# Optimization experiments

Hardware: AMD Instinct MI355X
Metric: run time of the kernel (lower is better)

Reference implementation:

```python
import jax, jax.numpy as jnp
import numpy as np

D = 256; NH = 8; NL = 4; NP = 4; HD = D // NH
SHAPES = [(128, 128), (64, 64), (32, 32), (16, 16)]
S = sum(h * w for h, w in SHAPES)  # 21760
B = 2; Q = 10000


def setup_inputs() -> dict:
    key = jax.random.key(0)
    ks = jax.random.split(key, 12)
    sc = 0.02
    return {
        "query": jax.random.normal(ks[0], (B, Q, D), jnp.float32),
        "ref_points": jax.random.uniform(ks[1], (B, Q, NL, 2), jnp.float32),
        "value": jax.random.normal(ks[2], (B, S, D), jnp.float32),
        "spatial_shapes": np.array(SHAPES, dtype=np.int64),
        "Wv": jax.random.normal(ks[3], (D, D), jnp.float32) * sc,
        "bv": jnp.zeros((D,), jnp.float32),
        "Ws": jax.random.normal(ks[4], (D, NH * NL * NP * 2), jnp.float32) * sc,
        "bs": jax.random.normal(ks[5], (NH * NL * NP * 2,), jnp.float32) * 0.5,
        "Wa": jax.random.normal(ks[6], (D, NH * NL * NP), jnp.float32) * sc,
        "ba": jnp.zeros((NH * NL * NP,), jnp.float32),
        "Wo": jax.random.normal(ks[7], (D, D), jnp.float32) * sc,
        "bo": jnp.zeros((D,), jnp.float32),
    }


def _ms_deform_attn(query, ref_points, value, shapes, Wv, bv, Ws, bs, Wa, ba, Wo, bo):
    Bn, Qn, _ = query.shape
    # value projection -> [B, NH, S, HD]
    v = (value @ Wv + bv).reshape(Bn, -1, NH, HD).transpose(0, 2, 1, 3)
    # sampling offsets [B,Q,NH,NL,NP,2] and softmax attn weights [B,Q,NH,NL,NP]
    off = (query @ Ws + bs).reshape(Bn, Qn, NH, NL, NP, 2)
    w = jax.nn.softmax((query @ Wa + ba).reshape(Bn, Qn, NH, NL * NP), axis=-1)
    w = w.reshape(Bn, Qn, NH, NL, NP)
    # per-level [w, h] normalizer (note original builds [[w,h] for h,w in shapes])
    norm = jnp.array([[wd, ht] for ht, wd in shapes], dtype=query.dtype)
    locs = ref_points[:, :, None, :, None, :] + off / norm[None, None, None, :, None, :]
    grids = (2.0 * locs - 1.0).transpose(0, 2, 1, 3, 4, 5)  # [B,NH,Q,NL,NP,2]
    wt = w.transpose(0, 2, 1, 3, 4)                          # [B,NH,Q,NL,NP]

    out = jnp.zeros((Bn, NH, Qn, HD), query.dtype)
    start = 0
    for lid, (h, wd) in enumerate(shapes):
        vl = v[:, :, start:start + h * wd, :]  # [B,NH,h*w,HD]
        g = grids[:, :, :, lid]                # [B,NH,Q,NP,2]
        # torch grid_sample align_corners=False pixel coords
        x = ((g[..., 0] + 1.0) * wd - 1.0) * 0.5
        y = ((g[..., 1] + 1.0) * h - 1.0) * 0.5
        x0f = jnp.floor(x); y0f = jnp.floor(y)
        lx = x - x0f; ly = y - y0f
        x0 = x0f.astype(jnp.int32); y0 = y0f.astype(jnp.int32)

        def samp(iy, ix):
            valid = ((iy >= 0) & (iy < h) & (ix >= 0) & (ix < wd)).astype(vl.dtype)
            idx = jnp.clip(iy, 0, h - 1) * wd + jnp.clip(ix, 0, wd - 1)  # [B,NH,Q,NP]
            flat = idx.reshape(Bn, NH, Qn * NP)
            gathered = jnp.take_along_axis(vl, flat[..., None], axis=2)
            return gathered.reshape(Bn, NH, Qn, NP, HD) * valid[..., None]

        s = (samp(y0, x0) * ((1 - lx) * (1 - ly))[..., None]
             + samp(y0, x0 + 1) * (lx * (1 - ly))[..., None]
             + samp(y0 + 1, x0) * ((1 - lx) * ly)[..., None]
             + samp(y0 + 1, x0 + 1) * (lx * ly)[..., None])
        out = out + jnp.einsum('bnqph,bnqp->bnqh', s, wt[:, :, :, lid])
        start += h * wd

    out = out.transpose(0, 2, 1, 3).reshape(Bn, Qn, D)
    return out @ Wo + bo


def reference(query, ref_points, value, spatial_shapes, Wv, bv, Ws, bs, Wa, ba, Wo, bo):
    shapes = [(int(h), int(w)) for h, w in np.asarray(spatial_shapes)]
    return _ms_deform_attn(query, ref_points, value, shapes, Wv, bv, Ws, bs, Wa, ba, Wo, bo)
```

## Files before the change

### kernel.cpp

```cpp
#include <hip/hip_runtime.h>

#define NB_B  2
#define NB_Q  10000
#define NB_D  256
#define NB_NH 8
#define NB_NL 4
#define NB_NP 4
#define NB_HD 32
#define NB_S  21760
#define MQ    20000
#define MQB   313
#define NVB   1360
#define NCB   939

#define ASTR  536
#define BSTR  1048

typedef _Float16 half8 __attribute__((ext_vector_type(8)));
typedef float f32x4 __attribute__((ext_vector_type(4)));

__global__ __launch_bounds__(256) void k_prepw(const float* __restrict__ Wv,
                                               const float* __restrict__ Ws,
                                               const float* __restrict__ Wa,
                                               const float* __restrict__ Wo,
                                               _Float16* __restrict__ Wvt,
                                               _Float16* __restrict__ Wsat,
                                               _Float16* __restrict__ Wot)
{
    const int k = threadIdx.x;
    const int nc = blockIdx.x;
    if (nc < 256) {
        Wvt[nc * 256 + k] = (_Float16)Wv[k * 256 + nc];
    } else if (nc < 640) {
        const int n = nc - 256;
        const float v = (n < 256) ? Ws[k * 256 + n] : Wa[k * 128 + (n - 256)];
        Wsat[n * 256 + k] = (_Float16)v;
    } else {
        const int n = nc - 640;
        Wot[n * 256 + k] = (_Float16)Wo[k * 256 + n];
    }
}

__global__ __launch_bounds__(256) void k_front(const float* __restrict__ value,
                                               const float* __restrict__ query,
                                               const _Float16* __restrict__ Wvt,
                                               const _Float16* __restrict__ Wsat,
                                               const float* __restrict__ refp,
                                               const float* __restrict__ bv,
                                               const float* __restrict__ bs,
                                               const float* __restrict__ ba,
                                               _Float16* __restrict__ vt,
                                               float* __restrict__ sx,
                                               float* __restrict__ sy,
                                               float* __restrict__ sw)
{
    __shared__ __align__(16) _Float16 Ah[2][4 * ASTR];
    __shared__ __align__(16) _Float16 Bh[2][4 * BSTR];
    __shared__ float rp[64][8];

    const int t = threadIdx.x;
    const int lane = t & 63, w = t >> 6;
    const int bid = blockIdx.x;
    const bool isv = (bid < NVB);

    int row0, n0;
    const float* Asrc;
    const _Float16* Bsrc;
    if (isv) {
        n0 = (bid & 1) * 128;
        row0 = (bid >> 1) * 64;
        Asrc = value;
        Bsrc = Wvt;
    } else {
        const int cid = bid - NVB;
        n0 = (cid % 3) * 128;
        row0 = (cid / 3) * 64;
        Asrc = query;
        Bsrc = Wsat;
        const int i0 = row0 * 8 + t;
        rp[t >> 3][t & 7] = refp[min(i0, MQ * 8 - 1)];
        const int i1 = i0 + 256;
        rp[32 + (t >> 3)][t & 7] = refp[min(i1, MQ * 8 - 1)];
    }

    const int arr = t >> 3;
    const int acl = t & 7;
    const int bnn = t >> 2;
    const int bcl = t & 3;

    const float* gA0;
    const float* gA1;
    {
        int r0i = row0 + arr, r1i = row0 + 32 + arr;
        if (!isv) { r0i = min(r0i, MQ - 1); r1i = min(r1i, MQ - 1); }
        gA0 = Asrc + (size_t)r0i * 256 + acl * 4;
        gA1 = Asrc + (size_t)r1i * 256 + acl * 4;
    }
    const _Float16* gB0 = Bsrc + (size_t)(n0 + bnn) * 256 + bcl * 8;
    const _Float16* gB1 = Bsrc + (size_t)(n0 + 64 + bnn) * 256 + bcl * 8;

    float4 ar0, ar1;
    uint4  br0, br1;
#define LOADT(kt) { ar0 = *reinterpret_cast<const float4*>(gA0 + (kt) * 32); \
                    ar1 = *reinterpret_cast<const float4*>(gA1 + (kt) * 32); \
                    br0 = *reinterpret_cast<const uint4*>(gB0 + (kt) * 32);  \
                    br1 = *reinterpret_cast<const uint4*>(gB1 + (kt) * 32); }

    LOADT(0);

    f32x4 acc[4][2];
#pragma unroll
    for (int fr = 0; fr < 4; ++fr)
#pragma unroll
        for (int fc = 0; fc < 2; ++fc) acc[fr][fc] = (f32x4){0.f, 0.f, 0.f, 0.f};

    const int rowb = lane & 15;
    const int kq = lane >> 4;
    const int awoff = (acl >> 1) * ASTR + arr * 8 + (acl & 1) * 4;
    int buf = 0;
#pragma unroll
    for (int kt = 0; kt < 8; ++kt) {
        {
            union { _Float16 h[4]; uint2 u; } p0, p1;
            p0.h[0] = (_Float16)ar0.x; p0.h[1] = (_Float16)ar0.y;
            p0.h[2] = (_Float16)ar0.z; p0.h[3] = (_Float16)ar0.w;
            p1.h[0] = (_Float16)ar1.x; p1.h[1] = (_Float16)ar1.y;
            p1.h[2] = (_Float16)ar1.z; p1.h[3] = (_Float16)ar1.w;
            *reinterpret_cast<uint2*>(&Ah[buf][awoff])           = p0.u;
            *reinterpret_cast<uint2*>(&Ah[buf][awoff + 32 * 8])  = p1.u;
            *reinterpret_cast<uint4*>(&Bh[buf][bcl * BSTR + bnn * 8])        = br0;
            *reinterpret_cast<uint4*>(&Bh[buf][bcl * BSTR + (64 + bnn) * 8]) = br1;
        }
        if (kt < 7) LOADT(kt + 1);
        __syncthreads();

        half8 af[4], bf[2];
#pragma unroll
        for (int fr = 0; fr < 4; ++fr)
            af[fr] = *reinterpret_cast<const half8*>(&Ah[buf][kq * ASTR + (fr * 16 + rowb) * 8]);
#pragma unroll
        for (int fc = 0; fc < 2; ++fc)
            bf[fc] = *reinterpret_cast<const half8*>(&Bh[buf][kq * BSTR + (w * 32 + fc * 16 + rowb) * 8]);
#pragma unroll
        for (int fr = 0; fr < 4; ++fr)
#pragma unroll
            for (int fc = 0; fc < 2; ++fc)
                acc[fr][fc] = __builtin_amdgcn_mfma_f32_16x16x32_f16(af[fr], bf[fc], acc[fr][fc], 0, 0, 0);
        buf ^= 1;
    }
#undef LOADT

    if (isv) {
        const int b = (row0 >= NB_S) ? 1 : 0;
        const int sb = row0 - b * NB_S;
#pragma unroll
        for (int fc = 0; fc < 2; ++fc) {
            const int n = n0 + w * 32 + fc * 16 + rowb;
            const int h = n >> 5, hd = n & 31;
            const float bvn = bv[n];
#pragma unroll
            for (int fr = 0; fr < 4; ++fr) {
                const f32x4 c = acc[fr][fc];
#pragma unroll
                for (int j = 0; j < 4; ++j) {
                    const int m = fr * 16 + (lane >> 4) * 4 + j;
                    vt[((size_t)((b * NB_NH + h) * NB_S + (sb + m)) << 5) + hd] = (_Float16)(c[j] + bvn);
                }
            }
        }
    } else if (n0 < 256) {
#pragma unroll
        for (int fc = 0; fc < 2; ++fc) {
            const int n = n0 + w * 32 + fc * 16 + rowb;
            const int si = n >> 1, xy = n & 1;
            const int l = (n >> 3) & 3;
            const float dim = (float)(128 >> l);
            const float bsv = bs[n];
            float* dst = xy ? sy : sx;
#pragma unroll
            for (int fr = 0; fr < 4; ++fr) {
                const f32x4 c = acc[fr][fc];
#pragma unroll
                for (int j = 0; j < 4; ++j) {
                    const int m = fr * 16 + (lane >> 4) * 4 + j;
                    if (row0 + m < MQ) {
                        const float coord = rp[m][l * 2 + xy] * dim + (c[j] + bsv) - 0.5f;
                        dst[(size_t)(row0 + m) * 128 + si] = coord;
                    }
                }
            }
        }
    } else {
#pragma unroll
        for (int fc = 0; fc < 2; ++fc) {
            const int col = w * 32 + fc * 16 + rowb;
            const float bav = ba[col];
#pragma unroll
            for (int fr = 0; fr < 4; ++fr) {
                const f32x4 c = acc[fr][fc];
#pragma unroll
                for (int j = 0; j < 4; ++j) {
                    const int m = fr * 16 + (lane >> 4) * 4 + j;
                    float v = c[j] + bav;
                    float vm = v;
                    vm = fmaxf(vm, __shfl_xor(vm, 1));
                    vm = fmaxf(vm, __shfl_xor(vm, 2));
                    vm = fmaxf(vm, __shfl_xor(vm, 4));
                    vm = fmaxf(vm, __shfl_xor(vm, 8));
                    const float e = expf(v - vm);
                    float s = e;
                    s += __shfl_xor(s, 1);
                    s += __shfl_xor(s, 2);
                    s += __shfl_xor(s, 4);
                    s += __shfl_xor(s, 8);
                    if (row0 + m < MQ)
                        sw[(size_t)(row0 + m) * 128 + col] = e / s;
                }
            }
        }
    }
}

__global__ __launch_bounds__(256) void k_gather(const _Float16* __restrict__ vt,
                                                const float* __restrict__ sx,
                                                const float* __restrict__ sy,
                                                const float* __restrict__ sw,
                                                _Float16* __restrict__ tmp)
{
    __shared__ int   offs[16][16][4];
    __shared__ float wts[16][16][4];
    const int t = threadIdx.x;
    const int gid = blockIdx.x;
    const int h = gid & 7;
    const int row0 = (gid >> 3) * 16;
    const int b = (row0 >= NB_Q) ? 1 : 0;

    {
        const int r = t >> 4, s = t & 15;
        const size_t ci = (size_t)(row0 + r) * 128 + h * 16 + s;
        const float x = sx[ci], y = sy[ci], w = sw[ci];
        const int l = s >> 2;
        const int dim = 128 >> l;
        const int startL = (l == 0) ? 0 : (l == 1) ? 16384 : (l == 2) ? 20480 : 21504;
        const float x0f = floorf(x), y0f = floorf(y);
        const float lx = x - x0f, ly = y - y0f;
        const int ix = (int)x0f, iy = (int)y0f;
        const int ix0 = min(max(ix, 0), dim - 1), ix1 = min(max(ix + 1, 0), dim - 1);
        const int iy0 = min(max(iy, 0), dim - 1), iy1 = min(max(iy + 1, 0), dim - 1);
        const float vx0 = (ix >= 0 && ix < dim) ? 1.f : 0.f;
        const float vx1 = (ix + 1 >= 0 && ix + 1 < dim) ? 1.f : 0.f;
        const float vy0 = (iy >= 0 && iy < dim) ? 1.f : 0.f;
        const float vy1 = (iy + 1 >= 0 && iy + 1 < dim) ? 1.f : 0.f;
        offs[r][s][0] = (startL + iy0 * dim + ix0) * (NB_HD * 2);
        offs[r][s][1] = (startL + iy0 * dim + ix1) * (NB_HD * 2);
        offs[r][s][2] = (startL + iy1 * dim + ix0) * (NB_HD * 2);
        offs[r][s][3] = (startL + iy1 * dim + ix1) * (NB_HD * 2);
        wts[r][s][0] = w * (1.f - lx) * (1.f - ly) * vx0 * vy0;
        wts[r][s][1] = w * lx * (1.f - ly) * vx1 * vy0;
        wts[r][s][2] = w * (1.f - lx) * ly * vx0 * vy1;
        wts[r][s][3] = w * lx * ly * vx1 * vy1;
    }
    __syncthreads();

    const int r = t >> 4, hd2 = t & 15;
    const char* slab = reinterpret_cast<const char*>(vt)
                     + (size_t)(b * NB_NH + h) * NB_S * (NB_HD * 2);
    const int byo = hd2 * 4;
    float ax = 0.f, ay = 0.f;
#pragma unroll
    for (int s = 0; s < 16; ++s) {
        const int4   o = *reinterpret_cast<const int4*>(&offs[r][s][0]);
        const float4 w = *reinterpret_cast<const float4*>(&wts[r][s][0]);
        union { unsigned u; _Float16 h[2]; } c0, c1, c2, c3;
        c0.u = *reinterpret_cast<const unsigned*>(slab + (o.x + byo));
        c1.u = *reinterpret_cast<const unsigned*>(slab + (o.y + byo));
        c2.u = *reinterpret_cast<const unsigned*>(slab + (o.z + byo));
        c3.u = *reinterpret_cast<const unsigned*>(slab + (o.w + byo));
        ax = fmaf(w.x, (float)c0.h[0], ax); ay = fmaf(w.x, (float)c0.h[1], ay);
        ax = fmaf(w.y, (float)c1.h[0], ax); ay = fmaf(w.y, (float)c1.h[1], ay);
        ax = fmaf(w.z, (float)c2.h[0], ax); ay = fmaf(w.z, (float)c2.h[1], ay);
        ax = fmaf(w.w, (float)c3.h[0], ax); ay = fmaf(w.w, (float)c3.h[1], ay);
    }
    union { unsigned u; _Float16 h[2]; } p;
    p.h[0] = (_Float16)ax; p.h[1] = (_Float16)ay;
    *reinterpret_cast<unsigned*>(tmp + (size_t)(row0 + r) * 256 + h * 32 + hd2 * 2) = p.u;
}

__global__ __launch_bounds__(256) void k_oproj_mm(const _Float16* __restrict__ tmp,
                                                  const _Float16* __restrict__ Wot,
                                                  const float* __restrict__ bo,
                                                  float* __restrict__ out)
{
    __shared__ __align__(16) _Float16 Ao[2][4 * ASTR];
    __shared__ __align__(16) _Float16 Bh[2][4 * BSTR];
    const int t = threadIdx.x;
    const int lane = t & 63, w = t >> 6;
    const int bid = blockIdx.x;
    const int n0 = (bid & 1) * 128;
    const int row0 = (bid >> 1) * 64;

    const int arr = t >> 2;
    const int acl = t & 3;
    const int bnn = t >> 2;
    const int bcl = t & 3;

    const _Float16* gA0 = tmp + (size_t)min(row0 + arr, MQ - 1) * 256 + acl * 8;
    const _Float16* gB0 = Wot + (size_t)(n0 + bnn) * 256 + bcl * 8;
    const _Float16* gB1 = Wot + (size_t)(n0 + 64 + bnn) * 256 + bcl * 8;

    uint4 ar0, br0, br1;
#define LOADT(kt) { ar0 = *reinterpret_cast<const uint4*>(gA0 + (kt) * 32); \
                    br0 = *reinterpret_cast<const uint4*>(gB0 + (kt) * 32); \
                    br1 = *reinterpret_cast<const uint4*>(gB1 + (kt) * 32); }

    LOADT(0);

    f32x4 acc[4][2];
#pragma unroll
    for (int fr = 0; fr < 4; ++fr)
#pragma unroll
        for (int fc = 0; fc < 2; ++fc) acc[fr][fc] = (f32x4){0.f, 0.f, 0.f, 0.f};

    const int rowb = lane & 15;
    const int kq = lane >> 4;
    int buf = 0;
#pragma unroll
    for (int kt = 0; kt < 8; ++kt) {
        *reinterpret_cast<uint4*>(&Ao[buf][acl * ASTR + arr * 8])            = ar0;
        *reinterpret_cast<uint4*>(&Bh[buf][bcl * BSTR + bnn * 8])            = br0;
        *reinterpret_cast<uint4*>(&Bh[buf][bcl * BSTR + (64 + bnn) * 8])     = br1;
        if (kt < 7) LOADT(kt + 1);
        __syncthreads();

        half8 af[4], bf[2];
#pragma unroll
        for (int fr = 0; fr < 4; ++fr)
            af[fr] = *reinterpret_cast<const half8*>(&Ao[buf][kq * ASTR + (fr * 16 + rowb) * 8]);
#pragma unroll
        for (int fc = 0; fc < 2; ++fc)
            bf[fc] = *reinterpret_cast<const half8*>(&Bh[buf][kq * BSTR + (w * 32 + fc * 16 + rowb) * 8]);
#pragma unroll
        for (int fr = 0; fr < 4; ++fr)
#pragma unroll
            for (int fc = 0; fc < 2; ++fc)
                acc[fr][fc] = __builtin_amdgcn_mfma_f32_16x16x32_f16(af[fr], bf[fc], acc[fr][fc], 0, 0, 0);
        buf ^= 1;
    }
#undef LOADT

#pragma unroll
    for (int fc = 0; fc < 2; ++fc) {
        const int n = n0 + w * 32 + fc * 16 + rowb;
        const float bon = bo[n];
#pragma unroll
        for (int fr = 0; fr < 4; ++fr) {
            const f32x4 c = acc[fr][fc];
#pragma unroll
            for (int j = 0; j < 4; ++j) {
                const int m = fr * 16 + (lane >> 4) * 4 + j;
                if (row0 + m < MQ)
                    out[(size_t)(row0 + m) * 256 + n] = c[j] + bon;
            }
        }
    }
}

extern "C" void kernel_launch(void* const* d_in, const int* in_sizes, int n_in,
                              void* d_out, int out_size, void* d_ws, size_t ws_size,
                              hipStream_t stream)
{
    const float* query = (const float*)d_in[0];
    const float* refp  = (const float*)d_in[1];
    const float* value = (const float*)d_in[2];
    const float* Wv = (const float*)d_in[4];
    const float* bv = (const float*)d_in[5];
    const float* Ws = (const float*)d_in[6];
    const float* bs = (const float*)d_in[7];
    const float* Wa = (const float*)d_in[8];
    const float* ba = (const float*)d_in[9];
    const float* Wo = (const float*)d_in[10];
    const float* bo = (const float*)d_in[11];
    float* out = (float*)d_out;

    char* ws = (char*)d_ws;
    _Float16* vt_h  = (_Float16*)(ws + 0);
    _Float16* tmp_h = (_Float16*)(ws + 22282240);
    _Float16* Wvt   = (_Float16*)(ws + 32522240);
    _Float16* Wsat  = (_Float16*)(ws + 32653312);
    _Float16* Wot   = (_Float16*)(ws + 32849920);
    float*    sxg   = (float*)   (ws + 32980992);
    float*    syg   = (float*)   (ws + 43220992);
    float*    swg   = (float*)   (ws + 53460992);

    hipLaunchKernelGGL(k_prepw, dim3(896), dim3(256), 0, stream,
                       Wv, Ws, Wa, Wo, Wvt, Wsat, Wot);
    hipLaunchKernelGGL(k_front, dim3(NVB + NCB), dim3(256), 0, stream,
                       value, query, Wvt, Wsat, refp, bv, bs, ba,
                       vt_h, sxg, syg, swg);
    hipLaunchKernelGGL(k_gather, dim3(NB_B * NB_Q / 16 * NB_NH), dim3(256), 0, stream,
                       vt_h, sxg, syg, swg, tmp_h);
    hipLaunchKernelGGL(k_oproj_mm, dim3(MQB * 2), dim3(256), 0, stream,
                       tmp_h, Wot, bo, out);
}
```

Baseline: 99.39 us.

## Deepen GEMM prefetch pipeline to two register stages in projection kernels

```diff
diff --git a/kernel.cpp b/kernel.cpp
--- a/kernel.cpp
+++ b/kernel.cpp
@@ -99,40 +99,44 @@
     const _Float16* gB0 = Bsrc + (size_t)(n0 + bnn) * 256 + bcl * 8;
     const _Float16* gB1 = Bsrc + (size_t)(n0 + 64 + bnn) * 256 + bcl * 8;
 
-    float4 ar0, ar1;
-    uint4  br0, br1;
-#define LOADT(kt) { ar0 = *reinterpret_cast<const float4*>(gA0 + (kt) * 32); \
-                    ar1 = *reinterpret_cast<const float4*>(gA1 + (kt) * 32); \
-                    br0 = *reinterpret_cast<const uint4*>(gB0 + (kt) * 32);  \
-                    br1 = *reinterpret_cast<const uint4*>(gB1 + (kt) * 32); }
-
-    LOADT(0);
+    float4 ar0[2], ar1[2];
+    uint4  br0[2], br1[2];
+#define LOADT(rs, kt) { ar0[rs] = *reinterpret_cast<const float4*>(gA0 + (kt) * 32); \
+                        ar1[rs] = *reinterpret_cast<const float4*>(gA1 + (kt) * 32); \
+                        br0[rs] = *reinterpret_cast<const uint4*>(gB0 + (kt) * 32);  \
+                        br1[rs] = *reinterpret_cast<const uint4*>(gB1 + (kt) * 32); }
+
+    const int awoff = (acl >> 1) * ASTR + arr * 8 + (acl & 1) * 4;
+#define WRITET(buf, rs) { \
+        union { _Float16 h[4]; uint2 u; } p0, p1; \
+        p0.h[0] = (_Float16)ar0[rs].x; p0.h[1] = (_Float16)ar0[rs].y; \
+        p0.h[2] = (_Float16)ar0[rs].z; p0.h[3] = (_Float16)ar0[rs].w; \
+        p1.h[0] = (_Float16)ar1[rs].x; p1.h[1] = (_Float16)ar1[rs].y; \
+        p1.h[2] = (_Float16)ar1[rs].z; p1.h[3] = (_Float16)ar1[rs].w; \
+        *reinterpret_cast<uint2*>(&Ah[buf][awoff])          = p0.u; \
+        *reinterpret_cast<uint2*>(&Ah[buf][awoff + 32 * 8]) = p1.u; \
+        *reinterpret_cast<uint4*>(&Bh[buf][bcl * BSTR + bnn * 8])        = br0[rs]; \
+        *reinterpret_cast<uint4*>(&Bh[buf][bcl * BSTR + (64 + bnn) * 8]) = br1[rs]; }
 
     f32x4 acc[4][2];
 #pragma unroll
     for (int fr = 0; fr < 4; ++fr)
 #pragma unroll
         for (int fc = 0; fc < 2; ++fc) acc[fr][fc] = (f32x4){0.f, 0.f, 0.f, 0.f};
+
+    LOADT(0, 0);
+    LOADT(1, 1);
+    WRITET(0, 0);
+    LOADT(0, 2);
+    __syncthreads();
 
     const int rowb = lane & 15;
     const int kq = lane >> 4;
-    const int awoff = (acl >> 1) * ASTR + arr * 8 + (acl & 1) * 4;
-    int buf = 0;
 #pragma unroll
     for (int kt = 0; kt < 8; ++kt) {
-        {
-            union { _Float16 h[4]; uint2 u; } p0, p1;
-            p0.h[0] = (_Float16)ar0.x; p0.h[1] = (_Float16)ar0.y;
-            p0.h[2] = (_Float16)ar0.z; p0.h[3] = (_Float16)ar0.w;
-            p1.h[0] = (_Float16)ar1.x; p1.h[1] = (_Float16)ar1.y;
-            p1.h[2] = (_Float16)ar1.z; p1.h[3] = (_Float16)ar1.w;
-            *reinterpret_cast<uint2*>(&Ah[buf][awoff])           = p0.u;
-            *reinterpret_cast<uint2*>(&Ah[buf][awoff + 32 * 8])  = p1.u;
-            *reinterpret_cast<uint4*>(&Bh[buf][bcl * BSTR + bnn * 8])        = br0;
-            *reinterpret_cast<uint4*>(&Bh[buf][bcl * BSTR + (64 + bnn) * 8]) = br1;
-        }
-        if (kt < 7) LOADT(kt + 1);
-        __syncthreads();
+        const int buf = kt & 1;
+        if (kt < 7) WRITET(buf ^ 1, (kt + 1) & 1);
+        if (kt < 5) LOADT((kt + 1) & 1, kt + 3);
 
         half8 af[4], bf[2];
 #pragma unroll
@@ -146,9 +150,10 @@
 #pragma unroll
             for (int fc = 0; fc < 2; ++fc)
                 acc[fr][fc] = __builtin_amdgcn_mfma_f32_16x16x32_f16(af[fr], bf[fc], acc[fr][fc], 0, 0, 0);
-        buf ^= 1;
+        if (kt < 7) __syncthreads();
     }
 #undef LOADT
+#undef WRITET
 
     if (isv) {
         const int b = (row0 >= NB_S) ? 1 : 0;
@@ -308,29 +313,34 @@
     const _Float16* gB0 = Wot + (size_t)(n0 + bnn) * 256 + bcl * 8;
     const _Float16* gB1 = Wot + (size_t)(n0 + 64 + bnn) * 256 + bcl * 8;
 
-    uint4 ar0, br0, br1;
-#define LOADT(kt) { ar0 = *reinterpret_cast<const uint4*>(gA0 + (kt) * 32); \
-                    br0 = *reinterpret_cast<const uint4*>(gB0 + (kt) * 32); \
-                    br1 = *reinterpret_cast<const uint4*>(gB1 + (kt) * 32); }
-
-    LOADT(0);
+    uint4 ar[2], br0[2], br1[2];
+#define LOADT(rs, kt) { ar[rs]  = *reinterpret_cast<const uint4*>(gA0 + (kt) * 32); \
+                        br0[rs] = *reinterpret_cast<const uint4*>(gB0 + (kt) * 32); \
+                        br1[rs] = *reinterpret_cast<const uint4*>(gB1 + (kt) * 32); }
+#define WRITET(buf, rs) { \
+        *reinterpret_cast<uint4*>(&Ao[buf][acl * ASTR + arr * 8])        = ar[rs]; \
+        *reinterpret_cast<uint4*>(&Bh[buf][bcl * BSTR + bnn * 8])        = br0[rs]; \
+        *reinterpret_cast<uint4*>(&Bh[buf][bcl * BSTR + (64 + bnn) * 8]) = br1[rs]; }
 
     f32x4 acc[4][2];
 #pragma unroll
     for (int fr = 0; fr < 4; ++fr)
 #pragma unroll
         for (int fc = 0; fc < 2; ++fc) acc[fr][fc] = (f32x4){0.f, 0.f, 0.f, 0.f};
+
+    LOADT(0, 0);
+    LOADT(1, 1);
+    WRITET(0, 0);
+    LOADT(0, 2);
+    __syncthreads();
 
     const int rowb = lane & 15;
     const int kq = lane >> 4;
-    int buf = 0;
 #pragma unroll
     for (int kt = 0; kt < 8; ++kt) {
-        *reinterpret_cast<uint4*>(&Ao[buf][acl * ASTR + arr * 8])            = ar0;
-        *reinterpret_cast<uint4*>(&Bh[buf][bcl * BSTR + bnn * 8])            = br0;
-        *reinterpret_cast<uint4*>(&Bh[buf][bcl * BSTR + (64 + bnn) * 8])     = br1;
-        if (kt < 7) LOADT(kt + 1);
-        __syncthreads();
+        const int buf = kt & 1;
+        if (kt < 7) WRITET(buf ^ 1, (kt + 1) & 1);
+        if (kt < 5) LOADT((kt + 1) & 1, kt + 3);
 
         half8 af[4], bf[2];
 #pragma unroll
@@ -344,9 +354,10 @@
 #pragma unroll
             for (int fc = 0; fc < 2; ++fc)
                 acc[fr][fc] = __builtin_amdgcn_mfma_f32_16x16x32_f16(af[fr], bf[fc], acc[fr][fc], 0, 0, 0);
-        buf ^= 1;
+        if (kt < 7) __syncthreads();
     }
 #undef LOADT
+#undef WRITET
 
 #pragma unroll
     for (int fc = 0; fc < 2; ++fc) {
```

New measurement: 145.8 us. +46.7%, slower.

## Widen front GEMM tiles to full N so each input row tile loads once

Applied to the files above, without the earlier changes.

```diff
diff --git a/kernel.cpp b/kernel.cpp
--- a/kernel.cpp
+++ b/kernel.cpp
@@ -10,11 +10,13 @@
 #define NB_S  21760
 #define MQ    20000
 #define MQB   313
-#define NVB   1360
-#define NCB   939
+#define NVB3  680
+#define NCO3  313
+#define NCL3  313
 
 #define ASTR  536
-#define BSTR  1048
+#define BSTR2 2056
+#define BSTRO 1048
 
 typedef _Float16 half8 __attribute__((ext_vector_type(8)));
 typedef float f32x4 __attribute__((ext_vector_type(4)));
@@ -55,28 +57,25 @@
                                                float* __restrict__ sw)
 {
     __shared__ __align__(16) _Float16 Ah[2][4 * ASTR];
-    __shared__ __align__(16) _Float16 Bh[2][4 * BSTR];
+    __shared__ __align__(16) _Float16 Bh[2][4 * BSTR2];
     __shared__ float rp[64][8];
 
     const int t = threadIdx.x;
     const int lane = t & 63, w = t >> 6;
     const int bid = blockIdx.x;
-    const bool isv = (bid < NVB);
-
-    int row0, n0;
+    const int type = (bid < NVB3) ? 0 : (bid < NVB3 + NCO3) ? 1 : 2;
+    const bool isv = (type == 0);
+
+    int row0;
     const float* Asrc;
     const _Float16* Bsrc;
-    if (isv) {
-        n0 = (bid & 1) * 128;
-        row0 = (bid >> 1) * 64;
-        Asrc = value;
-        Bsrc = Wvt;
-    } else {
-        const int cid = bid - NVB;
-        n0 = (cid % 3) * 128;
-        row0 = (cid / 3) * 64;
-        Asrc = query;
-        Bsrc = Wsat;
+    if (type == 0)      { row0 = bid * 64;                 Asrc = value; Bsrc = Wvt; }
+    else if (type == 1) { row0 = (bid - NVB3) * 64;        Asrc = query; Bsrc = Wsat; }
+    else                { row0 = (bid - NVB3 - NCO3) * 64; Asrc = query; Bsrc = Wsat + 256 * 256; }
+    const int nb  = (type == 2) ? 2 : 4;
+    const int nwd = (type == 2) ? 32 : 64;
+
+    if (type == 1) {
         const int i0 = row0 * 8 + t;
         rp[t >> 3][t & 7] = refp[min(i0, MQ * 8 - 1)];
         const int i1 = i0 + 256;
@@ -96,66 +95,71 @@
         gA0 = Asrc + (size_t)r0i * 256 + acl * 4;
         gA1 = Asrc + (size_t)r1i * 256 + acl * 4;
     }
-    const _Float16* gB0 = Bsrc + (size_t)(n0 + bnn) * 256 + bcl * 8;
-    const _Float16* gB1 = Bsrc + (size_t)(n0 + 64 + bnn) * 256 + bcl * 8;
+    const _Float16* gBb = Bsrc + (size_t)bnn * 256 + bcl * 8;
 
     float4 ar0, ar1;
-    uint4  br0, br1;
+    uint4  br[4];
 #define LOADT(kt) { ar0 = *reinterpret_cast<const float4*>(gA0 + (kt) * 32); \
                     ar1 = *reinterpret_cast<const float4*>(gA1 + (kt) * 32); \
-                    br0 = *reinterpret_cast<const uint4*>(gB0 + (kt) * 32);  \
-                    br1 = *reinterpret_cast<const uint4*>(gB1 + (kt) * 32); }
+                    _Pragma("unroll") \
+                    for (int i = 0; i < 4; ++i) \
+                        if (i < nb) br[i] = *reinterpret_cast<const uint4*>(gBb + (size_t)i * 64 * 256 + (kt) * 32); }
+
+    const int awoff = (acl >> 1) * ASTR + arr * 8 + (acl & 1) * 4;
+#define WRITET(buf) { \
+        union { _Float16 h[4]; uint2 u; } p0, p1; \
+        p0.h[0] = (_Float16)ar0.x; p0.h[1] = (_Float16)ar0.y; \
+        p0.h[2] = (_Float16)ar0.z; p0.h[3] = (_Float16)ar0.w; \
+        p1.h[0] = (_Float16)ar1.x; p1.h[1] = (_Float16)ar1.y; \
+        p1.h[2] = (_Float16)ar1.z; p1.h[3] = (_Float16)ar1.w; \
+        *reinterpret_cast<uint2*>(&Ah[buf][awoff])          = p0.u; \
+        *reinterpret_cast<uint2*>(&Ah[buf][awoff + 32 * 8]) = p1.u; \
+        _Pragma("unroll") \
+        for (int i = 0; i < 4; ++i) \
+            if (i < nb) *reinterpret_cast<uint4*>(&Bh[buf][bcl * BSTR2 + (i * 64 + bnn) * 8]) = br[i]; }
+
+    f32x4 acc[4][4];
+#pragma unroll
+    for (int fr = 0; fr < 4; ++fr)
+#pragma unroll
+        for (int fc = 0; fc < 4; ++fc) acc[fr][fc] = (f32x4){0.f, 0.f, 0.f, 0.f};
 
     LOADT(0);
-
-    f32x4 acc[4][2];
-#pragma unroll
-    for (int fr = 0; fr < 4; ++fr)
-#pragma unroll
-        for (int fc = 0; fc < 2; ++fc) acc[fr][fc] = (f32x4){0.f, 0.f, 0.f, 0.f};
 
     const int rowb = lane & 15;
     const int kq = lane >> 4;
-    const int awoff = (acl >> 1) * ASTR + arr * 8 + (acl & 1) * 4;
-    int buf = 0;
 #pragma unroll
     for (int kt = 0; kt < 8; ++kt) {
-        {
-            union { _Float16 h[4]; uint2 u; } p0, p1;
-            p0.h[0] = (_Float16)ar0.x; p0.h[1] = (_Float16)ar0.y;
-            p0.h[2] = (_Float16)ar0.z; p0.h[3] = (_Float16)ar0.w;
-            p1.h[0] = (_Float16)ar1.x; p1.h[1] = (_Float16)ar1.y;
-            p1.h[2] = (_Float16)ar1.z; p1.h[3] = (_Float16)ar1.w;
-            *reinterpret_cast<uint2*>(&Ah[buf][awoff])           = p0.u;
-            *reinterpret_cast<uint2*>(&Ah[buf][awoff + 32 * 8])  = p1.u;
-            *reinterpret_cast<uint4*>(&Bh[buf][bcl * BSTR + bnn * 8])        = br0;
-            *reinterpret_cast<uint4*>(&Bh[buf][bcl * BSTR + (64 + bnn) * 8]) = br1;
-        }
+        const int buf = kt & 1;
+        WRITET(buf);
         if (kt < 7) LOADT(kt + 1);
         __syncthreads();
 
-        half8 af[4], bf[2];
+        half8 af[4], bf[4];
 #pragma unroll
         for (int fr = 0; fr < 4; ++fr)
             af[fr] = *reinterpret_cast<const half8*>(&Ah[buf][kq * ASTR + (fr * 16 + rowb) * 8]);
 #pragma unroll
-        for (int fc = 0; fc < 2; ++fc)
-            bf[fc] = *reinterpret_cast<const half8*>(&Bh[buf][kq * BSTR + (w * 32 + fc * 16 + rowb) * 8]);
+        for (int fc = 0; fc < 4; ++fc)
+            if (fc * 16 < nwd)
+                bf[fc] = *reinterpret_cast<const half8*>(&Bh[buf][kq * BSTR2 + (w * nwd + fc * 16 + rowb) * 8]);
 #pragma unroll
         for (int fr = 0; fr < 4; ++fr)
 #pragma unroll
-            for (int fc = 0; fc < 2; ++fc)
-                acc[fr][fc] = __builtin_amdgcn_mfma_f32_16x16x32_f16(af[fr], bf[fc], acc[fr][fc], 0, 0, 0);
-        buf ^= 1;
+            for (int fc = 0; fc < 4; ++fc)
+                if (fc * 16 < nwd)
+                    acc[fr][fc] = __builtin_amdgcn_mfma_f32_16x16x32_f16(af[fr], bf[fc], acc[fr][fc], 0, 0, 0);
+        if (kt < 7) __syncthreads();
     }
 #undef LOADT
-
-    if (isv) {
+#undef WRITET
+
+    if (type == 0) {
         const int b = (row0 >= NB_S) ? 1 : 0;
         const int sb = row0 - b * NB_S;
 #pragma unroll
-        for (int fc = 0; fc < 2; ++fc) {
-            const int n = n0 + w * 32 + fc * 16 + rowb;
+        for (int fc = 0; fc < 4; ++fc) {
+            const int n = w * 64 + fc * 16 + rowb;
             const int h = n >> 5, hd = n & 31;
             const float bvn = bv[n];
 #pragma unroll
@@ -168,10 +172,10 @@
                 }
             }
         }
-    } else if (n0 < 256) {
-#pragma unroll
-        for (int fc = 0; fc < 2; ++fc) {
-            const int n = n0 + w * 32 + fc * 16 + rowb;
+    } else if (type == 1) {
+#pragma unroll
+        for (int fc = 0; fc < 4; ++fc) {
+            const int n = w * 64 + fc * 16 + rowb;
             const int si = n >> 1, xy = n & 1;
             const int l = (n >> 3) & 3;
             const float dim = (float)(128 >> l);
@@ -292,7 +296,7 @@
                                                   float* __restrict__ out)
 {
     __shared__ __align__(16) _Float16 Ao[2][4 * ASTR];
-    __shared__ __align__(16) _Float16 Bh[2][4 * BSTR];
+    __shared__ __align__(16) _Float16 Bh[2][4 * BSTRO];
     const int t = threadIdx.x;
     const int lane = t & 63, w = t >> 6;
     const int bid = blockIdx.x;
@@ -326,9 +330,9 @@
     int buf = 0;
 #pragma unroll
     for (int kt = 0; kt < 8; ++kt) {
-        *reinterpret_cast<uint4*>(&Ao[buf][acl * ASTR + arr * 8])            = ar0;
-        *reinterpret_cast<uint4*>(&Bh[buf][bcl * BSTR + bnn * 8])            = br0;
-        *reinterpret_cast<uint4*>(&Bh[buf][bcl * BSTR + (64 + bnn) * 8])     = br1;
+        *reinterpret_cast<uint4*>(&Ao[buf][acl * ASTR + arr * 8])        = ar0;
+        *reinterpret_cast<uint4*>(&Bh[buf][bcl * BSTRO + bnn * 8])        = br0;
+        *reinterpret_cast<uint4*>(&Bh[buf][bcl * BSTRO + (64 + bnn) * 8]) = br1;
         if (kt < 7) LOADT(kt + 1);
         __syncthreads();
 
@@ -338,7 +342,7 @@
             af[fr] = *reinterpret_cast<const half8*>(&Ao[buf][kq * ASTR + (fr * 16 + rowb) * 8]);
 #pragma unroll
         for (int fc = 0; fc < 2; ++fc)
-            bf[fc] = *reinterpret_cast<const half8*>(&Bh[buf][kq * BSTR + (w * 32 + fc * 16 + rowb) * 8]);
+            bf[fc] = *reinterpret_cast<const half8*>(&Bh[buf][kq * BSTRO + (w * 32 + fc * 16 + rowb) * 8]);
 #pragma unroll
         for (int fr = 0; fr < 4; ++fr)
 #pragma unroll
@@ -394,7 +398,7 @@
 
     hipLaunchKernelGGL(k_prepw, dim3(896), dim3(256), 0, stream,
                        Wv, Ws, Wa, Wo, Wvt, Wsat, Wot);
-    hipLaunchKernelGGL(k_front, dim3(NVB + NCB), dim3(256), 0, stream,
+    hipLaunchKernelGGL(k_front, dim3(NVB3 + NCO3 + NCL3), dim3(256), 0, stream,
                        value, query, Wvt, Wsat, refp, bv, bs, ba,
                        vt_h, sxg, syg, swg);
     hipLaunchKernelGGL(k_gather, dim3(NB_B * NB_Q / 16 * NB_NH), dim3(256), 0, stream,
```

New measurement: 129.7 us. 30.5% more time.
